# Kernel optimization log

Hardware: AMD Instinct MI355X
Metric: run time of the kernel (lower is better)

Reference implementation:

```python
import math
import jax, jax.numpy as jnp
import numpy as np

NEG = -1e10


def _rope_cos_sin(T, head_dim, dtype):
    # theta_i = 10000^(-2*(i-1)/dim), i=1..dim/2  ->  j=0..dim/2-1: 10000^(-2j/dim)
    j = jnp.arange(head_dim // 2, dtype=jnp.float32)
    inv_freq = 1.0 / (10000.0 ** (2.0 * j / head_dim))
    t = jnp.arange(T, dtype=jnp.float32)
    ang = t[:, None] * inv_freq[None, :]          # [T, hd/2]
    return jnp.cos(ang).astype(dtype), jnp.sin(ang).astype(dtype)


def _apply_rope(x, cos, sin):
    # x: [B, H, T, hd]; complex multiply (cos + i sin) * (x0 + i x1)
    B, H, T, hd = x.shape
    xr = x.reshape(B, H, T, hd // 2, 2)
    x0, x1 = xr[..., 0], xr[..., 1]
    c = cos[None, None]  # [1,1,T,hd/2]
    s = sin[None, None]
    o0 = c * x0 - s * x1
    o1 = s * x0 + c * x1
    return jnp.stack([o0, o1], axis=-1).reshape(B, H, T, hd)


def setup_inputs() -> dict:
    key = jax.random.key(0)
    ks = jax.random.split(key, 9)
    B, T, C = 2, 2048, 1024
    std = 0.02
    return {
        "x": jax.random.normal(ks[0], (B, T, C), jnp.float32),
        "Wq": jax.random.normal(ks[1], (C, C), jnp.float32) * std,
        "bq": jnp.zeros((C,), jnp.float32),
        "Wk": jax.random.normal(ks[2], (C, C), jnp.float32) * std,
        "bk": jnp.zeros((C,), jnp.float32),
        "Wv": jax.random.normal(ks[3], (C, C), jnp.float32) * std,
        "bv": jnp.zeros((C,), jnp.float32),
        "Wp": jax.random.normal(ks[4], (C, C), jnp.float32) * std,
        "bp": jnp.zeros((C,), jnp.float32),
    }


def reference(x, Wq, bq, Wk, bk, Wv, bv, Wp, bp):
    B, T, C = x.shape
    H = 16
    hd = C // H

    def heads(y):  # [B,T,C] -> [B,H,T,hd]
        return y.reshape(B, T, H, hd).transpose(0, 2, 1, 3)

    q = heads(x @ Wq.T + bq)
    k = heads(x @ Wk.T + bk)
    v = heads(x @ Wv.T + bv)

    cos, sin = _rope_cos_sin(T, hd, x.dtype)
    q = _apply_rope(q, cos, sin)
    k = _apply_rope(k, cos, sin)

    att = jnp.einsum('bhqd,bhkd->bhqk', q, k) * (1.0 / math.sqrt(hd))
    causal = jnp.tril(jnp.ones((T, T), bool))
    att = jnp.where(causal[None, None], att, jnp.asarray(NEG, att.dtype))
    att = jax.nn.softmax(att, axis=-1)

    y = jnp.einsum('bhqk,bhkd->bhqd', att, v)
    y = y.transpose(0, 2, 1, 3).reshape(B, T, C)
    return y @ Wp.T + bp
```

## Files before the change

### kernel.cpp

```cpp
#include <hip/hip_runtime.h>
#include <math.h>

typedef unsigned short u16;
typedef unsigned int u32;
typedef unsigned long long u64;
typedef __attribute__((ext_vector_type(8))) short short8;
typedef __attribute__((ext_vector_type(4))) float f32x4;
typedef __attribute__((ext_vector_type(4))) u16 u16x4;
typedef __attribute__((ext_vector_type(4))) u32 u32x4;

#define AS1 __attribute__((address_space(1)))
#define AS3 __attribute__((address_space(3)))

#define QSCALE 0.18033688011112042f

__device__ __forceinline__ u16 f2bf(float f) {
  union { float f; u32 i; } u; u.f = f;
  u32 r = u.i + 0x7FFFu + ((u.i >> 16) & 1u);
  return (u16)(r >> 16);
}

__device__ __forceinline__ u32 pk_bf16(float a, float b) {
  u32 r;
  asm volatile("v_cvt_pk_bf16_f32 %0, %1, %2" : "=v"(r) : "v"(a), "v"(b));
  return r;
}

__device__ __forceinline__ void gl_lds16(const void* g, void* l) {
  __builtin_amdgcn_global_load_lds((const AS1 u32*)g, (AS3 u32*)l, 16, 0, 0);
}

#define MFMA32(a, b, c) __builtin_amdgcn_mfma_f32_16x16x32_bf16(a, b, c, 0, 0, 0)

__global__ void cvt_all(const float* __restrict__ x,
                        const float* __restrict__ Wq, const float* __restrict__ Wk,
                        const float* __restrict__ Wv, const float* __restrict__ Wp,
                        u16* __restrict__ xb,
                        u16* __restrict__ Wqb, u16* __restrict__ Wkb,
                        u16* __restrict__ Wvb, u16* __restrict__ Wpb,
                        float* __restrict__ cosT, float* __restrict__ sinT,
                        int n4x, int n4tot) {
  int i = blockIdx.x * 256 + threadIdx.x;
  if (i >= n4tot) {
    int k = i - n4tot;
    int t = k >> 5, j = k & 31;
    float inv = powf(10000.0f, -(float)j / 32.0f);
    float ang = (float)t * inv;
    cosT[k] = cosf(ang);
    sinT[k] = sinf(ang);
    return;
  }
  const float* src; u16* dst; int off;
  if (i < n4x) { src = x; dst = xb; off = i; }
  else {
    int wi = i - n4x;
    int sel = wi >> 18;
    off = wi & ((1 << 18) - 1);
    src = sel == 0 ? Wq : sel == 1 ? Wk : sel == 2 ? Wv : Wp;
    dst = sel == 0 ? Wqb : sel == 1 ? Wkb : sel == 2 ? Wvb : Wpb;
  }
  float4 v = ((const float4*)src)[off];
  u16x4 o = { f2bf(v.x), f2bf(v.y), f2bf(v.z), f2bf(v.w) };
  ((u16x4*)dst)[off] = o;
}

__global__ __launch_bounds__(256, 3) void gemm_qkv(
    const u16* __restrict__ xb,
    const u16* __restrict__ Wqb, const u16* __restrict__ Wkb, const u16* __restrict__ Wvb,
    const float* __restrict__ bq, const float* __restrict__ bk, const float* __restrict__ bv,
    const float* __restrict__ cosT, const float* __restrict__ sinT,
    u16* __restrict__ Qb, u16* __restrict__ Kb, u16* __restrict__ Vb) {
  const int K = 1024, N = 1024;
  __shared__ __attribute__((aligned(16))) u16 As[128 * 64];
  __shared__ __attribute__((aligned(16))) u16 Bs[128 * 64];
  const int tid = threadIdx.x;
  const int lane = tid & 63;
  const int hi = lane >> 4, cc = lane & 15;
  const int w = tid >> 6, wm = w >> 1, wn = w & 1;

  const int lin = blockIdx.x + 24 * blockIdx.y;
  const int a_ = lin & 7;
  const int m_ = lin >> 3;
  const int c_ = a_ * 3 + (m_ % 3);
  const int sel = c_ >> 3;
  const int row0 = (m_ / 3) * 128, col0 = (c_ & 7) * 128;

  const u16* W = sel == 0 ? Wqb : sel == 1 ? Wkb : Wvb;
  const float* bias = sel == 0 ? bq : sel == 1 ? bk : bv;
  u16* Out = sel == 0 ? Qb : sel == 1 ? Kb : Vb;

  const int lr = tid >> 3;
  const int lkb = (((tid & 7) ^ (lr & 7)) * 8);
  const u16* Ag = xb + (size_t)(row0 + lr) * K + lkb;
  const u16* Wg = W + (size_t)(col0 + lr) * K + lkb;

  f32x4 acc[4][4];
#pragma unroll
  for (int m = 0; m < 4; ++m)
#pragma unroll
    for (int n = 0; n < 4; ++n) acc[m][n] = f32x4{0.f, 0.f, 0.f, 0.f};

  for (int k0 = 0; k0 < K; k0 += 64) {
    __syncthreads();
#pragma unroll
    for (int j = 0; j < 4; ++j) {
      gl_lds16(Ag + (size_t)j * 32 * K + k0, As + j * 2048 + tid * 8);
      gl_lds16(Wg + (size_t)j * 32 * K + k0, Bs + j * 2048 + tid * 8);
    }
    __syncthreads();
    short8 a[2][4], b[2][4];
#pragma unroll
    for (int kk = 0; kk < 2; ++kk) {
#pragma unroll
      for (int m = 0; m < 4; ++m)
        a[kk][m] = *(const short8*)(As + (wm * 64 + m * 16 + cc) * 64 +
                                    (((kk * 4 + hi) ^ (cc & 7)) * 8));
#pragma unroll
      for (int n = 0; n < 4; ++n)
        b[kk][n] = *(const short8*)(Bs + (wn * 64 + n * 16 + cc) * 64 +
                                    (((kk * 4 + hi) ^ (cc & 7)) * 8));
    }
#pragma unroll
    for (int kk = 0; kk < 2; ++kk)
#pragma unroll
      for (int m = 0; m < 4; ++m)
#pragma unroll
        for (int n = 0; n < 4; ++n)
          acc[m][n] = MFMA32(a[kk][m], b[kk][n], acc[m][n]);
  }

  if (sel < 2) {
    const float qs = (sel == 0) ? QSCALE : 1.0f;
#pragma unroll
    for (int n = 0; n < 4; ++n) {
      const int col = col0 + wn * 64 + n * 16 + cc;
      const int j = (col & 63) >> 1;
      const float bb = bias[col];
#pragma unroll
      for (int m = 0; m < 4; ++m) {
        const int rw = row0 + wm * 64 + m * 16 + hi * 4;
#pragma unroll
        for (int r = 0; r < 4; ++r) {
          const int row = rw + r;
          const int t = row & 2047;
          float v = acc[m][n][r] + bb;
          float pv = __shfl_xor(v, 1);
          float c = cosT[t * 32 + j], s = sinT[t * 32 + j];
          float oo = (cc & 1) ? (s * pv + c * v) : (c * v - s * pv);
          Out[(size_t)row * N + col] = f2bf(oo * qs);
        }
      }
    }
  } else {
#pragma unroll
    for (int n = 0; n < 4; ++n) {
      const int col = col0 + wn * 64 + n * 16 + cc;
      const float bb = bias[col];
#pragma unroll
      for (int m = 0; m < 4; ++m) {
        const int rw = row0 + wm * 64 + m * 16 + hi * 4;
#pragma unroll
        for (int r = 0; r < 4; ++r)
          Out[(size_t)(rw + r) * N + col] = f2bf(acc[m][n][r] + bb);
      }
    }
  }
}

__global__ __launch_bounds__(256, 3) void flash_mfma(
    const u16* __restrict__ Qb, const u16* __restrict__ Kb,
    const u16* __restrict__ Vb, u16* __restrict__ Yb) {
  const int T = 2048, C = 1024;
  __shared__ __attribute__((aligned(16))) u16 Ks[64 * 64];
  __shared__ __attribute__((aligned(16))) u16 Vt[64 * 64];
  __shared__ __attribute__((aligned(16))) u16 Ps[4][16 * 64];

  const int tid = threadIdx.x;
  const int lane = tid & 63;
  const int hi = lane >> 4, cc = lane & 15;
  const int hi4 = hi * 4;
  const int w = tid >> 6;

  const int lin = blockIdx.x + 16 * blockIdx.y;
  const int bh  = (lin & 7) * 4 + ((lin >> 3) & 3);
  const int qtA = lin >> 5;
  const int qtB = 31 - qtA;
  const size_t hbase = (size_t)(bh >> 4) * T * C + (size_t)(bh & 15) * 64;
  const int qA0w = qtA * 64 + w * 16;
  const int qB0w = qtB * 64 + w * 16;

  short8 qaA0, qaA1, qaB0, qaB1;
  {
    const u16* qp = Qb + hbase + (size_t)(qA0w + cc) * C + hi * 8;
    qaA0 = *(const short8*)qp;
    qaA1 = *(const short8*)(qp + 32);
    qp = Qb + hbase + (size_t)(qB0w + cc) * C + hi * 8;
    qaB0 = *(const short8*)qp;
    qaB1 = *(const short8*)(qp + 32);
  }

  f32x4 oA[4], oB[4];
#pragma unroll
  for (int nt = 0; nt < 4; ++nt) {
    oA[nt] = f32x4{0.f, 0.f, 0.f, 0.f};
    oB[nt] = f32x4{0.f, 0.f, 0.f, 0.f};
  }
  float mA = -1e30f, lA = 0.f, mB = -1e30f, lB = 0.f;

  const int krow = tid >> 2, kcol = (tid & 3) * 16;
  const int vd0 = (tid & 31) * 2, vkey0 = (tid >> 5) * 8;
  const u16* kgp = Kb + hbase + (size_t)krow * C + kcol;
  const u16* vgp = Vb + hbase + (size_t)vkey0 * C + vd0;

  short8 kr0, kr1;
  u32 vr_[8];

  auto LOADT = [&](int kt) {
    const size_t off = (size_t)(kt * 64) * C;
    kr0 = *(const short8*)(kgp + off);
    kr1 = *(const short8*)(kgp + off + 8);
#pragma unroll
    for (int j = 0; j < 8; ++j)
      vr_[j] = *(const u32*)(vgp + off + (size_t)j * C);
  };

  char* KsB = (char*)Ks;
  char* VtB = (char*)Vt;
  char* PsW = (char*)(Ps[w]);

  auto WRITET = [&]() {
    const int kb = krow * 128 + kcol * 2;
    const int ksw = (krow & 7) << 4;
    *(short8*)(KsB + (kb ^ ksw)) = kr0;
    *(short8*)(KsB + ((kb + 16) ^ ksw)) = kr1;
    u32 lo0 = (vr_[0] & 0xFFFFu) | (vr_[1] << 16);
    u32 lo1 = (vr_[2] & 0xFFFFu) | (vr_[3] << 16);
    u32 lo2 = (vr_[4] & 0xFFFFu) | (vr_[5] << 16);
    u32 lo3 = (vr_[6] & 0xFFFFu) | (vr_[7] << 16);
    u32 hh0 = (vr_[0] >> 16) | (vr_[1] & 0xFFFF0000u);
    u32 hh1 = (vr_[2] >> 16) | (vr_[3] & 0xFFFF0000u);
    u32 hh2 = (vr_[4] >> 16) | (vr_[5] & 0xFFFF0000u);
    u32 hh3 = (vr_[6] >> 16) | (vr_[7] & 0xFFFF0000u);
    const int d1 = vd0 + 1;
    u32x4 vlo = {lo0, lo1, lo2, lo3};
    u32x4 vhi = {hh0, hh1, hh2, hh3};
    *(u32x4*)(VtB + ((vd0 * 128 + vkey0 * 2) ^ ((vd0 & 7) << 4))) = vlo;
    *(u32x4*)(VtB + ((d1 * 128 + vkey0 * 2) ^ ((d1 & 7) << 4))) = vhi;
  };

  const int ksw2 = (cc & 7) << 4;

  auto QKT = [&](short8 (&kf)[4][2], const short8& qa0, const short8& qa1,
                 f32x4 (&s)[4]) {
#pragma unroll
    for (int nt = 0; nt < 4; ++nt) {
      f32x4 z = f32x4{0.f, 0.f, 0.f, 0.f};
      z = MFMA32(kf[nt][0], qa0, z);
      z = MFMA32(kf[nt][1], qa1, z);
      s[nt] = z;
    }
  };

  auto SM = [&](f32x4 (&s)[4], float& mrow, float& lsum, f32x4* o) {
    float tm = s[0][0];
#pragma unroll
    for (int nt = 0; nt < 4; ++nt)
#pragma unroll
      for (int r = 0; r < 4; ++r) tm = fmaxf(tm, s[nt][r]);
    tm = fmaxf(tm, __shfl_xor(tm, 16));
    tm = fmaxf(tm, __shfl_xor(tm, 32));
    const bool need = tm > mrow + 8.0f;
    float corr = 1.0f;
    if (need) { corr = exp2f(mrow - tm); mrow = tm; }
    float psum = 0.f;
#pragma unroll
    for (int nt = 0; nt < 4; ++nt) {
      float e0 = exp2f(s[nt][0] - mrow);
      float e1 = exp2f(s[nt][1] - mrow);
      float e2 = exp2f(s[nt][2] - mrow);
      float e3 = exp2f(s[nt][3] - mrow);
      psum += (e0 + e1) + (e2 + e3);
      u32 pr[2] = { pk_bf16(e0, e1), pk_bf16(e2, e3) };
      *(u64*)(PsW + ((cc * 128 + nt * 32 + hi * 8) ^ ksw2)) = *(const u64*)pr;
    }
    psum += __shfl_xor(psum, 16);
    psum += __shfl_xor(psum, 32);
    lsum = lsum * corr + psum;
    if (__any(need)) {
#pragma unroll
      for (int nt = 0; nt < 4; ++nt) o[nt] *= corr;
    }
  };

  auto MASK = [&](f32x4 (&s)[4]) {
    const int qloc = w * 16 + cc;
#pragma unroll
    for (int nt = 0; nt < 4; ++nt)
#pragma unroll
      for (int r = 0; r < 4; ++r)
        if (nt * 16 + hi4 + r > qloc) s[nt][r] = -1e30f;
  };

  auto PV = [&](short8 (&vf)[2][4], f32x4* o) {
#pragma unroll
    for (int kc = 0; kc < 2; ++kc) {
      short8 pa = *(const short8*)(PsW + ((cc * 128 + kc * 64 + hi * 16) ^ ksw2));
#pragma unroll
      for (int nt = 0; nt < 4; ++nt)
        o[nt] = MFMA32(vf[kc][nt], pa, o[nt]);
    }
  };

  LOADT(0);
  WRITET();
  LOADT(1);
  __syncthreads();

  for (int kt = 0; kt <= qtB; ++kt) {
    short8 kf[4][2];
#pragma unroll
    for (int nt = 0; nt < 4; ++nt) {
      const int kb = (nt * 16 + cc) * 128 + hi * 16;
      kf[nt][0] = *(const short8*)(KsB + (kb ^ ksw2));
      kf[nt][1] = *(const short8*)(KsB + ((kb + 64) ^ ksw2));
    }

    const bool actA = (kt <= qtA);
    f32x4 sB[4], sA[4];
    QKT(kf, qaB0, qaB1, sB);
    if (actA) QKT(kf, qaA0, qaA1, sA);
    if (kt == qtB) MASK(sB);
    if (actA && kt == qtA) MASK(sA);

    short8 vf[2][4];
#pragma unroll
    for (int kc = 0; kc < 2; ++kc)
#pragma unroll
      for (int nt = 0; nt < 4; ++nt)
        vf[kc][nt] = *(const short8*)(VtB + (((nt * 16 + cc) * 128 + kc * 64 + hi * 16) ^ ksw2));

    SM(sB, mB, lB, oB);
    PV(vf, oB);
    if (actA) {
      SM(sA, mA, lA, oA);
      PV(vf, oA);
    }

    if (kt < qtB) {
      __syncthreads();
      WRITET();
      if (kt + 1 < qtB) LOADT(kt + 2);
      __syncthreads();
    }
  }

  const float ivA = 1.0f / lA, ivB = 1.0f / lB;
#pragma unroll
  for (int nt = 0; nt < 4; ++nt) {
    u16x4 yA = { f2bf(oA[nt][0] * ivA), f2bf(oA[nt][1] * ivA),
                 f2bf(oA[nt][2] * ivA), f2bf(oA[nt][3] * ivA) };
    *(u16x4*)(Yb + hbase + (size_t)(qA0w + cc) * C + nt * 16 + hi4) = yA;
    u16x4 yB = { f2bf(oB[nt][0] * ivB), f2bf(oB[nt][1] * ivB),
                 f2bf(oB[nt][2] * ivB), f2bf(oB[nt][3] * ivB) };
    *(u16x4*)(Yb + hbase + (size_t)(qB0w + cc) * C + nt * 16 + hi4) = yB;
  }
}

__global__ __launch_bounds__(256, 2) void gemm_proj(
    const u16* __restrict__ A, const u16* __restrict__ W,
    const float* __restrict__ bias, float* __restrict__ Out) {
  const int K = 1024, N = 1024;
  __shared__ __attribute__((aligned(16))) u16 As[128 * 64];
  __shared__ __attribute__((aligned(16))) u16 Bs[64 * 64];
  const int tid = threadIdx.x;
  const int lane = tid & 63;
  const int hi = lane >> 4, cc = lane & 15;
  const int w = tid >> 6, wm = w >> 1, wn = w & 1;

  const int lin = blockIdx.x + 16 * blockIdx.y;
  const int colt = (lin & 7) * 2 + ((lin >> 3) & 1);
  const int row0 = (lin >> 4) * 128, col0 = colt * 64;

  const int lr = tid >> 3;
  const int lkb = (((tid & 7) ^ (lr & 7)) * 8);
  const u16* Ag = A + (size_t)(row0 + lr) * K + lkb;
  const u16* Wg = W + (size_t)(col0 + lr) * K + lkb;

  f32x4 acc[4][2];
#pragma unroll
  for (int m = 0; m < 4; ++m)
#pragma unroll
    for (int n = 0; n < 2; ++n) acc[m][n] = f32x4{0.f, 0.f, 0.f, 0.f};

  for (int k0 = 0; k0 < K; k0 += 64) {
    __syncthreads();
#pragma unroll
    for (int j = 0; j < 4; ++j)
      gl_lds16(Ag + (size_t)j * 32 * K + k0, As + j * 2048 + tid * 8);
#pragma unroll
    for (int j = 0; j < 2; ++j)
      gl_lds16(Wg + (size_t)j * 32 * K + k0, Bs + j * 2048 + tid * 8);
    __syncthreads();
    short8 a[2][4], b[2][2];
#pragma unroll
    for (int kk = 0; kk < 2; ++kk) {
#pragma unroll
      for (int m = 0; m < 4; ++m)
        a[kk][m] = *(const short8*)(As + (wm * 64 + m * 16 + cc) * 64 +
                                    (((kk * 4 + hi) ^ (cc & 7)) * 8));
#pragma unroll
      for (int n = 0; n < 2; ++n)
        b[kk][n] = *(const short8*)(Bs + (wn * 32 + n * 16 + cc) * 64 +
                                    (((kk * 4 + hi) ^ (cc & 7)) * 8));
    }
#pragma unroll
    for (int kk = 0; kk < 2; ++kk)
#pragma unroll
      for (int m = 0; m < 4; ++m)
#pragma unroll
        for (int n = 0; n < 2; ++n)
          acc[m][n] = MFMA32(a[kk][m], b[kk][n], acc[m][n]);
  }

#pragma unroll
  for (int n = 0; n < 2; ++n) {
    const int col = col0 + wn * 32 + n * 16 + cc;
    const float bb = bias[col];
#pragma unroll
    for (int m = 0; m < 4; ++m) {
      const int rw = row0 + wm * 64 + m * 16 + hi * 4;
#pragma unroll
      for (int r = 0; r < 4; ++r)
        Out[(size_t)(rw + r) * N + col] = acc[m][n][r] + bb;
    }
  }
}

extern "C" void kernel_launch(void* const* d_in, const int* in_sizes, int n_in,
                              void* d_out, int out_size, void* d_ws, size_t ws_size,
                              hipStream_t stream) {
  const float* x  = (const float*)d_in[0];
  const float* Wq = (const float*)d_in[1];
  const float* bq = (const float*)d_in[2];
  const float* Wk = (const float*)d_in[3];
  const float* bk = (const float*)d_in[4];
  const float* Wv = (const float*)d_in[5];
  const float* bv = (const float*)d_in[6];
  const float* Wp = (const float*)d_in[7];
  const float* bp = (const float*)d_in[8];
  float* out = (float*)d_out;

  const int B = 2, T = 2048, C = 1024;
  const int M = B * T;
  const size_t MC = (size_t)M * C;
  const size_t CC = (size_t)C * C;

  char* p = (char*)d_ws;
  u16* xb  = (u16*)p;  p += MC * 2;
  u16* Wqb = (u16*)p;  p += CC * 2;
  u16* Wkb = (u16*)p;  p += CC * 2;
  u16* Wvb = (u16*)p;  p += CC * 2;
  u16* Wpb = (u16*)p;  p += CC * 2;
  u16* Qbb = (u16*)p;  p += MC * 2;
  u16* Kbb = (u16*)p;  p += MC * 2;
  u16* Vbb = (u16*)p;  p += MC * 2;
  float* cosT = (float*)p; p += (size_t)T * 32 * 4;
  float* sinT = (float*)p; p += (size_t)T * 32 * 4;

  const int n4x = (int)(MC / 4);
  const int n4tot = n4x + 4 * (int)(CC / 4);
  const int ntot = n4tot + T * 32;
  cvt_all<<<(ntot + 255) / 256, 256, 0, stream>>>(x, Wq, Wk, Wv, Wp,
                                                  xb, Wqb, Wkb, Wvb, Wpb,
                                                  cosT, sinT, n4x, n4tot);

  dim3 gq(24, M / 128);
  gemm_qkv<<<gq, 256, 0, stream>>>(xb, Wqb, Wkb, Wvb, bq, bk, bv, cosT, sinT, Qbb, Kbb, Vbb);

  dim3 fg(16, B * 16);
  flash_mfma<<<fg, 256, 0, stream>>>(Qbb, Kbb, Vbb, xb);

  dim3 gp(C / 64, M / 128);
  gemm_proj<<<gp, 256, 0, stream>>>(xb, Wpb, bp, out);
}
```

Before: 120.6 us.

## Split paired query tiles across separate waves in 512-thread flash blocks

Each flash-attention block now runs 8 waves: four waves own query tile A and four own tile B, where previously each wave processed both tiles in sequence. This doubles the number of waves sharing each K/V tile load, halves the per-thread K/V staging loads, and reduces per-wave register state (one accumulator set). The cost is that A-waves sit idle at barriers after their causal range ends, and V fragments are now read from LDS inside the PV loop rather than preloaded.

```diff
diff --git a/kernel.cpp b/kernel.cpp
--- a/kernel.cpp
+++ b/kernel.cpp
@@ -7,6 +7,7 @@
 typedef __attribute__((ext_vector_type(8))) short short8;
 typedef __attribute__((ext_vector_type(4))) float f32x4;
 typedef __attribute__((ext_vector_type(4))) u16 u16x4;
+typedef __attribute__((ext_vector_type(2))) u32 u32x2;
 typedef __attribute__((ext_vector_type(4))) u32 u32x4;
 
 #define AS1 __attribute__((address_space(1)))
@@ -167,60 +168,55 @@
   }
 }
 
-__global__ __launch_bounds__(256, 3) void flash_mfma(
+__global__ __launch_bounds__(512, 4) void flash_mfma(
     const u16* __restrict__ Qb, const u16* __restrict__ Kb,
     const u16* __restrict__ Vb, u16* __restrict__ Yb) {
   const int T = 2048, C = 1024;
   __shared__ __attribute__((aligned(16))) u16 Ks[64 * 64];
   __shared__ __attribute__((aligned(16))) u16 Vt[64 * 64];
-  __shared__ __attribute__((aligned(16))) u16 Ps[4][16 * 64];
+  __shared__ __attribute__((aligned(16))) u16 Ps[8][16 * 64];
 
   const int tid = threadIdx.x;
   const int lane = tid & 63;
   const int hi = lane >> 4, cc = lane & 15;
   const int hi4 = hi * 4;
   const int w = tid >> 6;
+  const int wl = w & 3;
+  const int isB = w >> 2;
 
   const int lin = blockIdx.x + 16 * blockIdx.y;
   const int bh  = (lin & 7) * 4 + ((lin >> 3) & 3);
   const int qtA = lin >> 5;
   const int qtB = 31 - qtA;
+  const int qtW = isB ? qtB : qtA;
   const size_t hbase = (size_t)(bh >> 4) * T * C + (size_t)(bh & 15) * 64;
-  const int qA0w = qtA * 64 + w * 16;
-  const int qB0w = qtB * 64 + w * 16;
-
-  short8 qaA0, qaA1, qaB0, qaB1;
+  const int q0w = qtW * 64 + wl * 16;
+
+  short8 qa0, qa1;
   {
-    const u16* qp = Qb + hbase + (size_t)(qA0w + cc) * C + hi * 8;
-    qaA0 = *(const short8*)qp;
-    qaA1 = *(const short8*)(qp + 32);
-    qp = Qb + hbase + (size_t)(qB0w + cc) * C + hi * 8;
-    qaB0 = *(const short8*)qp;
-    qaB1 = *(const short8*)(qp + 32);
-  }
-
-  f32x4 oA[4], oB[4];
-#pragma unroll
-  for (int nt = 0; nt < 4; ++nt) {
-    oA[nt] = f32x4{0.f, 0.f, 0.f, 0.f};
-    oB[nt] = f32x4{0.f, 0.f, 0.f, 0.f};
-  }
-  float mA = -1e30f, lA = 0.f, mB = -1e30f, lB = 0.f;
-
-  const int krow = tid >> 2, kcol = (tid & 3) * 16;
-  const int vd0 = (tid & 31) * 2, vkey0 = (tid >> 5) * 8;
+    const u16* qp = Qb + hbase + (size_t)(q0w + cc) * C + hi * 8;
+    qa0 = *(const short8*)qp;
+    qa1 = *(const short8*)(qp + 32);
+  }
+
+  f32x4 o[4];
+#pragma unroll
+  for (int nt = 0; nt < 4; ++nt) o[nt] = f32x4{0.f, 0.f, 0.f, 0.f};
+  float mrow = -1e30f, lsum = 0.f;
+
+  const int krow = tid >> 3, kcol = (tid & 7) * 8;
+  const int vd0 = (tid & 31) * 2, vkey0 = (tid >> 5) * 4;
   const u16* kgp = Kb + hbase + (size_t)krow * C + kcol;
   const u16* vgp = Vb + hbase + (size_t)vkey0 * C + vd0;
 
-  short8 kr0, kr1;
-  u32 vr_[8];
+  short8 kr0;
+  u32 vr_[4];
 
   auto LOADT = [&](int kt) {
     const size_t off = (size_t)(kt * 64) * C;
     kr0 = *(const short8*)(kgp + off);
-    kr1 = *(const short8*)(kgp + off + 8);
-#pragma unroll
-    for (int j = 0; j < 8; ++j)
+#pragma unroll
+    for (int j = 0; j < 4; ++j)
       vr_[j] = *(const u32*)(vgp + off + (size_t)j * C);
   };
 
@@ -232,84 +228,18 @@
     const int kb = krow * 128 + kcol * 2;
     const int ksw = (krow & 7) << 4;
     *(short8*)(KsB + (kb ^ ksw)) = kr0;
-    *(short8*)(KsB + ((kb + 16) ^ ksw)) = kr1;
     u32 lo0 = (vr_[0] & 0xFFFFu) | (vr_[1] << 16);
     u32 lo1 = (vr_[2] & 0xFFFFu) | (vr_[3] << 16);
-    u32 lo2 = (vr_[4] & 0xFFFFu) | (vr_[5] << 16);
-    u32 lo3 = (vr_[6] & 0xFFFFu) | (vr_[7] << 16);
     u32 hh0 = (vr_[0] >> 16) | (vr_[1] & 0xFFFF0000u);
     u32 hh1 = (vr_[2] >> 16) | (vr_[3] & 0xFFFF0000u);
-    u32 hh2 = (vr_[4] >> 16) | (vr_[5] & 0xFFFF0000u);
-    u32 hh3 = (vr_[6] >> 16) | (vr_[7] & 0xFFFF0000u);
     const int d1 = vd0 + 1;
-    u32x4 vlo = {lo0, lo1, lo2, lo3};
-    u32x4 vhi = {hh0, hh1, hh2, hh3};
-    *(u32x4*)(VtB + ((vd0 * 128 + vkey0 * 2) ^ ((vd0 & 7) << 4))) = vlo;
-    *(u32x4*)(VtB + ((d1 * 128 + vkey0 * 2) ^ ((d1 & 7) << 4))) = vhi;
+    u32x2 vlo = {lo0, lo1};
+    u32x2 vhi = {hh0, hh1};
+    *(u32x2*)(VtB + ((vd0 * 128 + vkey0 * 2) ^ ((vd0 & 7) << 4))) = vlo;
+    *(u32x2*)(VtB + ((d1 * 128 + vkey0 * 2) ^ ((d1 & 7) << 4))) = vhi;
   };
 
   const int ksw2 = (cc & 7) << 4;
-
-  auto QKT = [&](short8 (&kf)[4][2], const short8& qa0, const short8& qa1,
-                 f32x4 (&s)[4]) {
-#pragma unroll
-    for (int nt = 0; nt < 4; ++nt) {
-      f32x4 z = f32x4{0.f, 0.f, 0.f, 0.f};
-      z = MFMA32(kf[nt][0], qa0, z);
-      z = MFMA32(kf[nt][1], qa1, z);
-      s[nt] = z;
-    }
-  };
-
-  auto SM = [&](f32x4 (&s)[4], float& mrow, float& lsum, f32x4* o) {
-    float tm = s[0][0];
-#pragma unroll
-    for (int nt = 0; nt < 4; ++nt)
-#pragma unroll
-      for (int r = 0; r < 4; ++r) tm = fmaxf(tm, s[nt][r]);
-    tm = fmaxf(tm, __shfl_xor(tm, 16));
-    tm = fmaxf(tm, __shfl_xor(tm, 32));
-    const bool need = tm > mrow + 8.0f;
-    float corr = 1.0f;
-    if (need) { corr = exp2f(mrow - tm); mrow = tm; }
-    float psum = 0.f;
-#pragma unroll
-    for (int nt = 0; nt < 4; ++nt) {
-      float e0 = exp2f(s[nt][0] - mrow);
-      float e1 = exp2f(s[nt][1] - mrow);
-      float e2 = exp2f(s[nt][2] - mrow);
-      float e3 = exp2f(s[nt][3] - mrow);
-      psum += (e0 + e1) + (e2 + e3);
-      u32 pr[2] = { pk_bf16(e0, e1), pk_bf16(e2, e3) };
-      *(u64*)(PsW + ((cc * 128 + nt * 32 + hi * 8) ^ ksw2)) = *(const u64*)pr;
-    }
-    psum += __shfl_xor(psum, 16);
-    psum += __shfl_xor(psum, 32);
-    lsum = lsum * corr + psum;
-    if (__any(need)) {
-#pragma unroll
-      for (int nt = 0; nt < 4; ++nt) o[nt] *= corr;
-    }
-  };
-
-  auto MASK = [&](f32x4 (&s)[4]) {
-    const int qloc = w * 16 + cc;
-#pragma unroll
-    for (int nt = 0; nt < 4; ++nt)
-#pragma unroll
-      for (int r = 0; r < 4; ++r)
-        if (nt * 16 + hi4 + r > qloc) s[nt][r] = -1e30f;
-  };
-
-  auto PV = [&](short8 (&vf)[2][4], f32x4* o) {
-#pragma unroll
-    for (int kc = 0; kc < 2; ++kc) {
-      short8 pa = *(const short8*)(PsW + ((cc * 128 + kc * 64 + hi * 16) ^ ksw2));
-#pragma unroll
-      for (int nt = 0; nt < 4; ++nt)
-        o[nt] = MFMA32(vf[kc][nt], pa, o[nt]);
-    }
-  };
 
   LOADT(0);
   WRITET();
@@ -317,33 +247,72 @@
   __syncthreads();
 
   for (int kt = 0; kt <= qtB; ++kt) {
-    short8 kf[4][2];
-#pragma unroll
-    for (int nt = 0; nt < 4; ++nt) {
-      const int kb = (nt * 16 + cc) * 128 + hi * 16;
-      kf[nt][0] = *(const short8*)(KsB + (kb ^ ksw2));
-      kf[nt][1] = *(const short8*)(KsB + ((kb + 64) ^ ksw2));
-    }
-
-    const bool actA = (kt <= qtA);
-    f32x4 sB[4], sA[4];
-    QKT(kf, qaB0, qaB1, sB);
-    if (actA) QKT(kf, qaA0, qaA1, sA);
-    if (kt == qtB) MASK(sB);
-    if (actA && kt == qtA) MASK(sA);
-
-    short8 vf[2][4];
-#pragma unroll
-    for (int kc = 0; kc < 2; ++kc)
+    const bool act = (kt <= qtW);
+    if (act) {
+      short8 kf[4][2];
+#pragma unroll
+      for (int nt = 0; nt < 4; ++nt) {
+        const int kb = (nt * 16 + cc) * 128 + hi * 16;
+        kf[nt][0] = *(const short8*)(KsB + (kb ^ ksw2));
+        kf[nt][1] = *(const short8*)(KsB + ((kb + 64) ^ ksw2));
+      }
+
+      f32x4 s[4];
+#pragma unroll
+      for (int nt = 0; nt < 4; ++nt) {
+        f32x4 z = f32x4{0.f, 0.f, 0.f, 0.f};
+        z = MFMA32(kf[nt][0], qa0, z);
+        z = MFMA32(kf[nt][1], qa1, z);
+        s[nt] = z;
+      }
+
+      if (kt == qtW) {
+        const int qloc = wl * 16 + cc;
+#pragma unroll
+        for (int nt = 0; nt < 4; ++nt)
+#pragma unroll
+          for (int r = 0; r < 4; ++r)
+            if (nt * 16 + hi4 + r > qloc) s[nt][r] = -1e30f;
+      }
+
+      float tm = s[0][0];
 #pragma unroll
       for (int nt = 0; nt < 4; ++nt)
-        vf[kc][nt] = *(const short8*)(VtB + (((nt * 16 + cc) * 128 + kc * 64 + hi * 16) ^ ksw2));
-
-    SM(sB, mB, lB, oB);
-    PV(vf, oB);
-    if (actA) {
-      SM(sA, mA, lA, oA);
-      PV(vf, oA);
+#pragma unroll
+        for (int r = 0; r < 4; ++r) tm = fmaxf(tm, s[nt][r]);
+      tm = fmaxf(tm, __shfl_xor(tm, 16));
+      tm = fmaxf(tm, __shfl_xor(tm, 32));
+      const bool need = tm > mrow + 8.0f;
+      float corr = 1.0f;
+      if (need) { corr = exp2f(mrow - tm); mrow = tm; }
+      float psum = 0.f;
+#pragma unroll
+      for (int nt = 0; nt < 4; ++nt) {
+        float e0 = exp2f(s[nt][0] - mrow);
+        float e1 = exp2f(s[nt][1] - mrow);
+        float e2 = exp2f(s[nt][2] - mrow);
+        float e3 = exp2f(s[nt][3] - mrow);
+        psum += (e0 + e1) + (e2 + e3);
+        u32 pr[2] = { pk_bf16(e0, e1), pk_bf16(e2, e3) };
+        *(u64*)(PsW + ((cc * 128 + nt * 32 + hi * 8) ^ ksw2)) = *(const u64*)pr;
+      }
+      psum += __shfl_xor(psum, 16);
+      psum += __shfl_xor(psum, 32);
+      lsum = lsum * corr + psum;
+      if (__any(need)) {
+#pragma unroll
+        for (int nt = 0; nt < 4; ++nt) o[nt] *= corr;
+      }
+
+#pragma unroll
+      for (int kc = 0; kc < 2; ++kc) {
+        short8 pa = *(const short8*)(PsW + ((cc * 128 + kc * 64 + hi * 16) ^ ksw2));
+#pragma unroll
+        for (int nt = 0; nt < 4; ++nt) {
+          short8 vb = *(const short8*)(VtB + (((nt * 16 + cc) * 128 + kc * 64 + hi * 16) ^ ksw2));
+          o[nt] = MFMA32(vb, pa, o[nt]);
+        }
+      }
     }
 
     if (kt < qtB) {
@@ -354,15 +323,12 @@
     }
   }
 
-  const float ivA = 1.0f / lA, ivB = 1.0f / lB;
+  const float ivl = 1.0f / lsum;
 #pragma unroll
   for (int nt = 0; nt < 4; ++nt) {
-    u16x4 yA = { f2bf(oA[nt][0] * ivA), f2bf(oA[nt][1] * ivA),
-                 f2bf(oA[nt][2] * ivA), f2bf(oA[nt][3] * ivA) };
-    *(u16x4*)(Yb + hbase + (size_t)(qA0w + cc) * C + nt * 16 + hi4) = yA;
-    u16x4 yB = { f2bf(oB[nt][0] * ivB), f2bf(oB[nt][1] * ivB),
-                 f2bf(oB[nt][2] * ivB), f2bf(oB[nt][3] * ivB) };
-    *(u16x4*)(Yb + hbase + (size_t)(qB0w + cc) * C + nt * 16 + hi4) = yB;
+    u16x4 y = { f2bf(o[nt][0] * ivl), f2bf(o[nt][1] * ivl),
+                f2bf(o[nt][2] * ivl), f2bf(o[nt][3] * ivl) };
+    *(u16x4*)(Yb + hbase + (size_t)(q0w + cc) * C + nt * 16 + hi4) = y;
   }
 }
 
@@ -478,7 +444,7 @@
   gemm_qkv<<<gq, 256, 0, stream>>>(xb, Wqb, Wkb, Wvb, bq, bk, bv, cosT, sinT, Qbb, Kbb, Vbb);
 
   dim3 fg(16, B * 16);
-  flash_mfma<<<fg, 256, 0, stream>>>(Qbb, Kbb, Vbb, xb);
+  flash_mfma<<<fg, 512, 0, stream>>>(Qbb, Kbb, Vbb, xb);
 
   dim3 gp(C / 64, M / 128);
   gemm_proj<<<gp, 256, 0, stream>>>(xb, Wpb, bp, out);
```

New measurement: 114.7 us. 4.9% less time.
